# Kernel tuning notes

Hardware: AMD Instinct MI355X
Metric: run time of the kernel (lower is better)

## Reference

```python
import jax, jax.numpy as jnp
import numpy as np


def _gather_neighbours(h, idx):
    # h: (B, N, H); idx: (B, N, K) int -> (B, N, K, H)
    B, N, H = h.shape
    K = idx.shape[-1]
    flat = idx.reshape(B, N * K)  # (B, N*K)
    rep = jnp.take_along_axis(h, flat[..., None], axis=1)  # (B, N*K, H)
    return rep.reshape(B, N, K, H)


def _masked_agg(h, idx, mask):
    # gather neighbor hidden states then masked sum over neighbors -> (B, N, H)
    rep = _gather_neighbours(h, idx)
    return jnp.einsum('bnkh,bnk->bnh', rep, mask)


def setup_inputs() -> dict:
    key = jax.random.key(0)
    ks = jax.random.split(key, 12)
    B, N, H, K = 8, 2000, 128, 32
    s = 1.0 / np.sqrt(H)
    return {
        'node_hidden': jax.random.normal(ks[0], (B, N, H), jnp.float32),
        'cell': jax.random.normal(ks[1], (B, N, H), jnp.float32),
        'w_in': jax.random.normal(ks[2], (4, H, H), jnp.float32) * s,
        'w_out': jax.random.normal(ks[3], (4, H, H), jnp.float32) * s,
        'u_in': jax.random.normal(ks[4], (4, H, H), jnp.float32) * s,
        'u_out': jax.random.normal(ks[5], (4, H, H), jnp.float32) * s,
        'b': jax.random.normal(ks[6], (4, H), jnp.float32) * 0.1,
        'in_node_mask': jax.random.uniform(ks[7], (B, N, K), jnp.float32),
        'out_node_mask': jax.random.uniform(ks[8], (B, N, K), jnp.float32),
        'in_node_index': jax.random.randint(ks[9], (B, N, K), 0, N, jnp.int32),
        'out_node_index': jax.random.randint(ks[10], (B, N, K), 0, N, jnp.int32),
        'layer_num': 2,
    }


def reference(node_hidden, cell, w_in, w_out, u_in, u_out, b,
              in_node_mask, out_node_mask, in_node_index, out_node_index,
              layer_num):
    h, c = node_hidden, cell
    for _ in range(layer_num):
        in_agg = _masked_agg(h, in_node_index, in_node_mask)    # (B,N,H)
        out_agg = _masked_agg(h, out_node_index, out_node_mask)  # (B,N,H)
        # gate pre-activations, gate order: i, o, f, cell
        pre = (jnp.einsum('bnh,ghd->gbnd', in_agg, w_in)
               + jnp.einsum('bnh,ghd->gbnd', out_agg, w_out)
               + jnp.einsum('bnh,ghd->gbnd', h, u_in)
               + jnp.einsum('bnh,ghd->gbnd', h, u_out)
               + b[:, None, None, :])
        i_g = jax.nn.sigmoid(pre[0])
        o_g = jax.nn.sigmoid(pre[1])
        f_g = jax.nn.sigmoid(pre[2])
        g = jnp.tanh(pre[3])
        c = f_g * c + i_g * g
        h = o_g * jnp.tanh(c)
    return h
```

## Files before the change

kernel.cpp:

```cpp
#include <hip/hip_runtime.h>
#include <math.h>

#define B_ 8
#define N_ 2000
#define H_ 128
#define K_ 32
#define M_ (B_*N_)
#define KTOT 384
#define NC 512
#define NTILES 32
#define NCHUNK 12
#define ACHUNK 8

typedef __attribute__((ext_vector_type(8))) short s8_t;
typedef __attribute__((ext_vector_type(4))) float f4_t;

__device__ __forceinline__ unsigned short f2bf(float x) {
    union { float f; unsigned u; } v; v.f = x;
    unsigned r = v.u + 0x7fff + ((v.u >> 16) & 1);
    return (unsigned short)(r >> 16);
}
__device__ __forceinline__ float bf2f(unsigned short b) {
    union { unsigned u; float f; } v; v.u = (unsigned)b << 16; return v.f;
}
__device__ __forceinline__ float sigm_(float x) { return 1.f / (1.f + __expf(-x)); }
__device__ __forceinline__ float tanh_(float x) { return 2.f / (1.f + __expf(-2.f * x)) - 1.f; }

__device__ __forceinline__ float pickv(f4_t A, int m) {
    float ab = (m & 1) ? A.y : A.x;
    float cd = (m & 1) ? A.w : A.z;
    return (m & 2) ? cd : ab;
}
__device__ __forceinline__ float pick4(float u0, float u1, float u2, float u3, int m) {
    float ab = (m & 1) ? u1 : u0;
    float cd = (m & 1) ? u3 : u2;
    return (m & 2) ? cd : ab;
}

__global__ __launch_bounds__(512)
void prep_kernel(const float* __restrict__ w_in,
                 const float* __restrict__ w_out,
                 const float* __restrict__ u_in,
                 const float* __restrict__ u_out,
                 unsigned short* __restrict__ wp_hi,
                 unsigned short* __restrict__ wp_lo) {
    int blk = blockIdx.x;
    int ntile = blk / NCHUNK, chunk = blk % NCHUNK;
    int t = threadIdx.x;
    int lane = t >> 3, e = t & 7;
    int col = ntile * 16 + (lane & 15);
    int k = chunk * 32 + (lane >> 4) * 8 + e;
    int d = col >> 2, g = col & 3;
    float v;
    if (k < 128) {
        v = w_in[(g * 128 + k) * 128 + d];
    } else if (k < 256) {
        v = w_out[(g * 128 + (k - 128)) * 128 + d];
    } else {
        int kk = k - 256;
        v = u_in[(g * 128 + kk) * 128 + d] + u_out[(g * 128 + kk) * 128 + d];
    }
    unsigned short hs = f2bf(v);
    wp_hi[(size_t)blk * 512 + t] = hs;
    wp_lo[(size_t)blk * 512 + t] = f2bf(v - bf2f(hs));
}

__global__ __launch_bounds__(256)
void agg_kernel(const float* __restrict__ h,
                const int* __restrict__ in_idx,
                const float* __restrict__ in_mask,
                const int* __restrict__ out_idx,
                const float* __restrict__ out_mask,
                unsigned short* __restrict__ A_hi,
                unsigned short* __restrict__ A_lo) {
    int tid = threadIdx.x;
    int r = tid >> 5;
    int p = tid & 31;
    int row = blockIdx.x * 8 + r;
    int b = row / N_;
    const float* hb = h + (size_t)b * N_ * H_;

    __shared__ int   s_idx[8][64];
    __shared__ float s_msk[8][64];
    for (int e = tid; e < 512; e += 256) {
        int r2 = e >> 6, q = e & 63;
        int ridx = blockIdx.x * 8 + r2;
        if (q < 32) {
            s_idx[r2][q] = in_idx[ridx * K_ + q];
            s_msk[r2][q] = in_mask[ridx * K_ + q];
        } else {
            s_idx[r2][q] = out_idx[ridx * K_ + (q - 32)];
            s_msk[r2][q] = out_mask[ridx * K_ + (q - 32)];
        }
    }
    __syncthreads();

    int d0 = p * 4;
    float ai[4] = {0.f, 0.f, 0.f, 0.f};
    float ao[4] = {0.f, 0.f, 0.f, 0.f};
    #pragma unroll 4
    for (int k = 0; k < K_; ++k) {
        int   i1 = s_idx[r][k];
        float m1 = s_msk[r][k];
        int   i2 = s_idx[r][32 + k];
        float m2 = s_msk[r][32 + k];
        float4 v1 = *(const float4*)(hb + (size_t)i1 * H_ + d0);
        float4 v2 = *(const float4*)(hb + (size_t)i2 * H_ + d0);
        ai[0] += m1 * v1.x; ai[1] += m1 * v1.y; ai[2] += m1 * v1.z; ai[3] += m1 * v1.w;
        ao[0] += m2 * v2.x; ao[1] += m2 * v2.y; ao[2] += m2 * v2.z; ao[3] += m2 * v2.w;
    }

    int mtile = row >> 4;
    int kg = (p >> 1) & 3;
    int e0 = (p & 1) * 4;
    int lane = (row & 15) + 16 * kg;
    size_t bi = ((size_t)(mtile * ACHUNK + (p >> 3)) * 64 + lane) * 8 + e0;
    size_t bo = ((size_t)(mtile * ACHUNK + 4 + (p >> 3)) * 64 + lane) * 8 + e0;

    ushort4 hi_i, lo_i, hi_o, lo_o;
    {
        unsigned short h0 = f2bf(ai[0]), h1 = f2bf(ai[1]), h2 = f2bf(ai[2]), h3 = f2bf(ai[3]);
        hi_i = make_ushort4(h0, h1, h2, h3);
        lo_i = make_ushort4(f2bf(ai[0] - bf2f(h0)), f2bf(ai[1] - bf2f(h1)),
                            f2bf(ai[2] - bf2f(h2)), f2bf(ai[3] - bf2f(h3)));
        unsigned short g0 = f2bf(ao[0]), g1 = f2bf(ao[1]), g2 = f2bf(ao[2]), g3 = f2bf(ao[3]);
        hi_o = make_ushort4(g0, g1, g2, g3);
        lo_o = make_ushort4(f2bf(ao[0] - bf2f(g0)), f2bf(ao[1] - bf2f(g1)),
                            f2bf(ao[2] - bf2f(g2)), f2bf(ao[3] - bf2f(g3)));
    }
    *(ushort4*)(A_hi + bi) = hi_i;
    *(ushort4*)(A_lo + bi) = lo_i;
    *(ushort4*)(A_hi + bo) = hi_o;
    *(ushort4*)(A_lo + bo) = lo_o;
}

__global__ __launch_bounds__(256, 4)
void gemm_gates(const unsigned short* __restrict__ A_hi,
                const unsigned short* __restrict__ A_lo,
                const float* __restrict__ h_src,
                const unsigned short* __restrict__ wp_hi,
                const unsigned short* __restrict__ wp_lo,
                const float* __restrict__ bias,
                const float* __restrict__ c_src,
                float* __restrict__ c_dst,
                float* __restrict__ h_dst,
                int write_c) {
    int tid  = threadIdx.x;
    int mt   = blockIdx.x;
    int jt   = blockIdx.y;
    int lane = tid & 63;
    int w    = tid >> 6;
    int row0 = mt * 64;
    int m_off = (w & 1) * 32;
    int n_off = (w >> 1) * 64;
    int ml = lane & 15;
    int kg = lane >> 4;

    int mtile0 = mt * 4 + (w & 1) * 2;
    int ntile0 = jt * 8 + (w >> 1) * 4;

    f4_t zero = {0.f, 0.f, 0.f, 0.f};
    f4_t acc[2][4];
    #pragma unroll
    for (int i = 0; i < 2; ++i)
        #pragma unroll
        for (int j = 0; j < 4; ++j) acc[i][j] = zero;

    #pragma unroll 1
    for (int c = 0; c < ACHUNK; ++c) {
        s8_t a_hi[2], a_lo[2], b_hi[4], b_lo[4];
        #pragma unroll
        for (int i = 0; i < 2; ++i) {
            size_t off = ((size_t)((mtile0 + i) * ACHUNK + c) * 64 + lane) * 8;
            a_hi[i] = *(const s8_t*)(A_hi + off);
            a_lo[i] = *(const s8_t*)(A_lo + off);
        }
        #pragma unroll
        for (int j = 0; j < 4; ++j) {
            size_t boff = ((size_t)((ntile0 + j) * NCHUNK + c) * 64 + lane) * 8;
            b_hi[j] = *(const s8_t*)(wp_hi + boff);
            b_lo[j] = *(const s8_t*)(wp_lo + boff);
        }
        #pragma unroll
        for (int i = 0; i < 2; ++i)
            #pragma unroll
            for (int j = 0; j < 4; ++j) {
                acc[i][j] = __builtin_amdgcn_mfma_f32_16x16x32_bf16(a_hi[i], b_hi[j], acc[i][j], 0, 0, 0);
                acc[i][j] = __builtin_amdgcn_mfma_f32_16x16x32_bf16(a_hi[i], b_lo[j], acc[i][j], 0, 0, 0);
                acc[i][j] = __builtin_amdgcn_mfma_f32_16x16x32_bf16(a_lo[i], b_hi[j], acc[i][j], 0, 0, 0);
            }
    }

    #pragma unroll 1
    for (int c = ACHUNK; c < NCHUNK; ++c) {
        s8_t a_hi[2], a_lo[2], b_hi[4], b_lo[4];
        #pragma unroll
        for (int i = 0; i < 2; ++i) {
            const float* ph = h_src + (size_t)(row0 + m_off + i * 16 + ml) * H_
                              + (c - ACHUNK) * 32 + kg * 8;
            float4 f0 = *(const float4*)ph;
            float4 f1 = *(const float4*)(ph + 4);
            float fv[8] = {f0.x, f0.y, f0.z, f0.w, f1.x, f1.y, f1.z, f1.w};
            s8_t hv, lv;
            #pragma unroll
            for (int e = 0; e < 8; ++e) {
                unsigned short hs = f2bf(fv[e]);
                hv[e] = (short)hs;
                lv[e] = (short)f2bf(fv[e] - bf2f(hs));
            }
            a_hi[i] = hv;
            a_lo[i] = lv;
        }
        #pragma unroll
        for (int j = 0; j < 4; ++j) {
            size_t boff = ((size_t)((ntile0 + j) * NCHUNK + c) * 64 + lane) * 8;
            b_hi[j] = *(const s8_t*)(wp_hi + boff);
            b_lo[j] = *(const s8_t*)(wp_lo + boff);
        }
        #pragma unroll
        for (int i = 0; i < 2; ++i)
            #pragma unroll
            for (int j = 0; j < 4; ++j) {
                acc[i][j] = __builtin_amdgcn_mfma_f32_16x16x32_bf16(a_hi[i], b_hi[j], acc[i][j], 0, 0, 0);
                acc[i][j] = __builtin_amdgcn_mfma_f32_16x16x32_bf16(a_hi[i], b_lo[j], acc[i][j], 0, 0, 0);
                acc[i][j] = __builtin_amdgcn_mfma_f32_16x16x32_bf16(a_lo[i], b_hi[j], acc[i][j], 0, 0, 0);
            }
    }

    int g    = lane & 3;
    int qrow = lane >> 4;
    int dl   = (lane >> 2) & 3;
    #pragma unroll
    for (int j = 0; j < 4; ++j) {
        int ncol_base = jt * 128 + n_off + j * 16;
        int d = (ncol_base >> 2) + dl;
        float b0 = bias[0 * 128 + d];
        float b1 = bias[1 * 128 + d];
        float b2 = bias[2 * 128 + d];
        float b3 = bias[3 * 128 + d];
        #pragma unroll
        for (int i = 0; i < 2; ++i) {
            f4_t A = acc[i][j];
            float s0 = pickv(A, g);
            float s1 = pickv(A, g ^ 1);
            float s2 = pickv(A, g ^ 2);
            float s3 = pickv(A, g ^ 3);
            float u0 = s0;
            float u1 = __shfl_xor(s1, 1);
            float u2 = __shfl_xor(s2, 2);
            float u3 = __shfl_xor(s3, 3);
            float p0 = pick4(u0, u1, u2, u3, g) + b0;
            float p1 = pick4(u0, u1, u2, u3, g ^ 1) + b1;
            float p2 = pick4(u0, u1, u2, u3, g ^ 2) + b2;
            float p3 = pick4(u0, u1, u2, u3, g ^ 3) + b3;
            float ig = sigm_(p0);
            float og = sigm_(p1);
            float fg = sigm_(p2);
            float cg = tanh_(p3);
            int row = row0 + m_off + i * 16 + qrow * 4 + g;
            size_t off = (size_t)row * H_ + d;
            float c_old = c_src[off];
            float c_new = fg * c_old + ig * cg;
            if (write_c) c_dst[off] = c_new;
            h_dst[off] = og * tanh_(c_new);
        }
    }
}

extern "C" void kernel_launch(void* const* d_in, const int* in_sizes, int n_in,
                              void* d_out, int out_size, void* d_ws, size_t ws_size,
                              hipStream_t stream) {
    const float* node_hidden = (const float*)d_in[0];
    const float* cell        = (const float*)d_in[1];
    const float* w_in        = (const float*)d_in[2];
    const float* w_out       = (const float*)d_in[3];
    const float* u_in        = (const float*)d_in[4];
    const float* u_out       = (const float*)d_in[5];
    const float* bias        = (const float*)d_in[6];
    const float* in_mask     = (const float*)d_in[7];
    const float* out_mask    = (const float*)d_in[8];
    const int*   in_idx      = (const int*)d_in[9];
    const int*   out_idx     = (const int*)d_in[10];
    float* out = (float*)d_out;

    char* p = (char*)d_ws;
    unsigned short* wp_hi = (unsigned short*)p; p += (size_t)NTILES * NCHUNK * 512 * 2;
    unsigned short* wp_lo = (unsigned short*)p; p += (size_t)NTILES * NCHUNK * 512 * 2;
    unsigned short* A_hi  = (unsigned short*)p; p += (size_t)(M_/16) * ACHUNK * 512 * 2;
    unsigned short* A_lo  = (unsigned short*)p; p += (size_t)(M_/16) * ACHUNK * 512 * 2;
    float* h_buf = (float*)p;                   p += (size_t)M_ * H_ * 4;

    prep_kernel<<<NTILES * NCHUNK, 512, 0, stream>>>(w_in, w_out, u_in, u_out, wp_hi, wp_lo);

    agg_kernel<<<M_ / 8, 256, 0, stream>>>(node_hidden, in_idx, in_mask,
                                           out_idx, out_mask, A_hi, A_lo);
    gemm_gates<<<dim3(M_ / 64, 4), 256, 0, stream>>>(
        A_hi, A_lo, node_hidden, wp_hi, wp_lo, bias, cell, out, h_buf, 1);

    agg_kernel<<<M_ / 8, 256, 0, stream>>>(h_buf, in_idx, in_mask,
                                           out_idx, out_mask, A_hi, A_lo);
    gemm_gates<<<dim3(M_ / 64, 4), 256, 0, stream>>>(
        A_hi, A_lo, h_buf, wp_hi, wp_lo, bias, out, out, out, 0);
}
```

Measured before the change: 210.0 us.

## Pre-split h into packed A operand and double-buffer GEMM loads

The aggregation kernel now also converts each node's own hidden state into the packed bf16 hi/lo A layout, so the GEMM reads all 12 K-chunks from one packed buffer instead of converting fp32 h inline. The GEMM loop is fully unrolled with two register buffers so the next chunk's loads are issued before the current chunk's MFMAs, and the occupancy hint in launch_bounds is dropped. The aggregation block index is also remapped (blockIdx & 7) * 250 + (blockIdx >> 3), which spreads consecutive blocks across batches, presumably to balance gather traffic across XCD caches. The cost is a larger packed A buffer written and read through memory, and more registers per GEMM thread.

New measurement: 207.2 us. Within noise of the previous version (-1.4%).

```diff
diff --git a/kernel.cpp b/kernel.cpp
--- a/kernel.cpp
+++ b/kernel.cpp
@@ -10,7 +10,6 @@
 #define NC 512
 #define NTILES 32
 #define NCHUNK 12
-#define ACHUNK 8
 
 typedef __attribute__((ext_vector_type(8))) short s8_t;
 typedef __attribute__((ext_vector_type(4))) float f4_t;
@@ -35,6 +34,13 @@
     float ab = (m & 1) ? u1 : u0;
     float cd = (m & 1) ? u3 : u2;
     return (m & 2) ? cd : ab;
+}
+
+__device__ __forceinline__ void split4(const float* f, ushort4& hi, ushort4& lo) {
+    unsigned short h0 = f2bf(f[0]), h1 = f2bf(f[1]), h2 = f2bf(f[2]), h3 = f2bf(f[3]);
+    hi = make_ushort4(h0, h1, h2, h3);
+    lo = make_ushort4(f2bf(f[0] - bf2f(h0)), f2bf(f[1] - bf2f(h1)),
+                      f2bf(f[2] - bf2f(h2)), f2bf(f[3] - bf2f(h3)));
 }
 
 __global__ __launch_bounds__(512)
@@ -73,10 +79,11 @@
                 const float* __restrict__ out_mask,
                 unsigned short* __restrict__ A_hi,
                 unsigned short* __restrict__ A_lo) {
+    int bid = (blockIdx.x & 7) * 250 + (blockIdx.x >> 3);
     int tid = threadIdx.x;
     int r = tid >> 5;
     int p = tid & 31;
-    int row = blockIdx.x * 8 + r;
+    int row = bid * 8 + r;
     int b = row / N_;
     const float* hb = h + (size_t)b * N_ * H_;
 
@@ -84,7 +91,7 @@
     __shared__ float s_msk[8][64];
     for (int e = tid; e < 512; e += 256) {
         int r2 = e >> 6, q = e & 63;
-        int ridx = blockIdx.x * 8 + r2;
+        int ridx = bid * 8 + r2;
         if (q < 32) {
             s_idx[r2][q] = in_idx[ridx * K_ + q];
             s_msk[r2][q] = in_mask[ridx * K_ + q];
@@ -109,35 +116,26 @@
         ai[0] += m1 * v1.x; ai[1] += m1 * v1.y; ai[2] += m1 * v1.z; ai[3] += m1 * v1.w;
         ao[0] += m2 * v2.x; ao[1] += m2 * v2.y; ao[2] += m2 * v2.z; ao[3] += m2 * v2.w;
     }
+    float4 hv4 = *(const float4*)(h + (size_t)row * H_ + d0);
+    float hh[4] = {hv4.x, hv4.y, hv4.z, hv4.w};
 
     int mtile = row >> 4;
     int kg = (p >> 1) & 3;
     int e0 = (p & 1) * 4;
     int lane = (row & 15) + 16 * kg;
-    size_t bi = ((size_t)(mtile * ACHUNK + (p >> 3)) * 64 + lane) * 8 + e0;
-    size_t bo = ((size_t)(mtile * ACHUNK + 4 + (p >> 3)) * 64 + lane) * 8 + e0;
-
-    ushort4 hi_i, lo_i, hi_o, lo_o;
-    {
-        unsigned short h0 = f2bf(ai[0]), h1 = f2bf(ai[1]), h2 = f2bf(ai[2]), h3 = f2bf(ai[3]);
-        hi_i = make_ushort4(h0, h1, h2, h3);
-        lo_i = make_ushort4(f2bf(ai[0] - bf2f(h0)), f2bf(ai[1] - bf2f(h1)),
-                            f2bf(ai[2] - bf2f(h2)), f2bf(ai[3] - bf2f(h3)));
-        unsigned short g0 = f2bf(ao[0]), g1 = f2bf(ao[1]), g2 = f2bf(ao[2]), g3 = f2bf(ao[3]);
-        hi_o = make_ushort4(g0, g1, g2, g3);
-        lo_o = make_ushort4(f2bf(ao[0] - bf2f(g0)), f2bf(ao[1] - bf2f(g1)),
-                            f2bf(ao[2] - bf2f(g2)), f2bf(ao[3] - bf2f(g3)));
-    }
-    *(ushort4*)(A_hi + bi) = hi_i;
-    *(ushort4*)(A_lo + bi) = lo_i;
-    *(ushort4*)(A_hi + bo) = hi_o;
-    *(ushort4*)(A_lo + bo) = lo_o;
-}
-
-__global__ __launch_bounds__(256, 4)
+    size_t bi = ((size_t)(mtile * NCHUNK +     (p >> 3)) * 64 + lane) * 8 + e0;
+    size_t bo = ((size_t)(mtile * NCHUNK + 4 + (p >> 3)) * 64 + lane) * 8 + e0;
+    size_t bh = ((size_t)(mtile * NCHUNK + 8 + (p >> 3)) * 64 + lane) * 8 + e0;
+
+    ushort4 hi, lo;
+    split4(ai, hi, lo); *(ushort4*)(A_hi + bi) = hi; *(ushort4*)(A_lo + bi) = lo;
+    split4(ao, hi, lo); *(ushort4*)(A_hi + bo) = hi; *(ushort4*)(A_lo + bo) = lo;
+    split4(hh, hi, lo); *(ushort4*)(A_hi + bh) = hi; *(ushort4*)(A_lo + bh) = lo;
+}
+
+__global__ __launch_bounds__(256)
 void gemm_gates(const unsigned short* __restrict__ A_hi,
                 const unsigned short* __restrict__ A_lo,
-                const float* __restrict__ h_src,
                 const unsigned short* __restrict__ wp_hi,
                 const unsigned short* __restrict__ wp_lo,
                 const float* __restrict__ bias,
@@ -153,11 +151,16 @@
     int row0 = mt * 64;
     int m_off = (w & 1) * 32;
     int n_off = (w >> 1) * 64;
-    int ml = lane & 15;
-    int kg = lane >> 4;
 
     int mtile0 = mt * 4 + (w & 1) * 2;
     int ntile0 = jt * 8 + (w >> 1) * 4;
+
+    const unsigned short* pa0 = A_hi + ((size_t)mtile0 * NCHUNK * 64 + lane) * 8;
+    const unsigned short* pa1 = A_lo + ((size_t)mtile0 * NCHUNK * 64 + lane) * 8;
+    const unsigned short* pb0 = wp_hi + ((size_t)ntile0 * NCHUNK * 64 + lane) * 8;
+    const unsigned short* pb1 = wp_lo + ((size_t)ntile0 * NCHUNK * 64 + lane) * 8;
+    const size_t mstride = (size_t)NCHUNK * 512;
+    const size_t cstride = 512;
 
     f4_t zero = {0.f, 0.f, 0.f, 0.f};
     f4_t acc[2][4];
@@ -166,66 +169,45 @@
         #pragma unroll
         for (int j = 0; j < 4; ++j) acc[i][j] = zero;
 
-    #pragma unroll 1
-    for (int c = 0; c < ACHUNK; ++c) {
-        s8_t a_hi[2], a_lo[2], b_hi[4], b_lo[4];
-        #pragma unroll
-        for (int i = 0; i < 2; ++i) {
-            size_t off = ((size_t)((mtile0 + i) * ACHUNK + c) * 64 + lane) * 8;
-            a_hi[i] = *(const s8_t*)(A_hi + off);
-            a_lo[i] = *(const s8_t*)(A_lo + off);
-        }
-        #pragma unroll
-        for (int j = 0; j < 4; ++j) {
-            size_t boff = ((size_t)((ntile0 + j) * NCHUNK + c) * 64 + lane) * 8;
-            b_hi[j] = *(const s8_t*)(wp_hi + boff);
-            b_lo[j] = *(const s8_t*)(wp_lo + boff);
-        }
-        #pragma unroll
-        for (int i = 0; i < 2; ++i)
-            #pragma unroll
-            for (int j = 0; j < 4; ++j) {
-                acc[i][j] = __builtin_amdgcn_mfma_f32_16x16x32_bf16(a_hi[i], b_hi[j], acc[i][j], 0, 0, 0);
-                acc[i][j] = __builtin_amdgcn_mfma_f32_16x16x32_bf16(a_hi[i], b_lo[j], acc[i][j], 0, 0, 0);
-                acc[i][j] = __builtin_amdgcn_mfma_f32_16x16x32_bf16(a_lo[i], b_hi[j], acc[i][j], 0, 0, 0);
-            }
-    }
-
-    #pragma unroll 1
-    for (int c = ACHUNK; c < NCHUNK; ++c) {
-        s8_t a_hi[2], a_lo[2], b_hi[4], b_lo[4];
-        #pragma unroll
-        for (int i = 0; i < 2; ++i) {
-            const float* ph = h_src + (size_t)(row0 + m_off + i * 16 + ml) * H_
-                              + (c - ACHUNK) * 32 + kg * 8;
-            float4 f0 = *(const float4*)ph;
-            float4 f1 = *(const float4*)(ph + 4);
-            float fv[8] = {f0.x, f0.y, f0.z, f0.w, f1.x, f1.y, f1.z, f1.w};
-            s8_t hv, lv;
-            #pragma unroll
-            for (int e = 0; e < 8; ++e) {
-                unsigned short hs = f2bf(fv[e]);
-                hv[e] = (short)hs;
-                lv[e] = (short)f2bf(fv[e] - bf2f(hs));
-            }
-            a_hi[i] = hv;
-            a_lo[i] = lv;
-        }
-        #pragma unroll
-        for (int j = 0; j < 4; ++j) {
-            size_t boff = ((size_t)((ntile0 + j) * NCHUNK + c) * 64 + lane) * 8;
-            b_hi[j] = *(const s8_t*)(wp_hi + boff);
-            b_lo[j] = *(const s8_t*)(wp_lo + boff);
-        }
-        #pragma unroll
-        for (int i = 0; i < 2; ++i)
-            #pragma unroll
-            for (int j = 0; j < 4; ++j) {
-                acc[i][j] = __builtin_amdgcn_mfma_f32_16x16x32_bf16(a_hi[i], b_hi[j], acc[i][j], 0, 0, 0);
-                acc[i][j] = __builtin_amdgcn_mfma_f32_16x16x32_bf16(a_hi[i], b_lo[j], acc[i][j], 0, 0, 0);
-                acc[i][j] = __builtin_amdgcn_mfma_f32_16x16x32_bf16(a_lo[i], b_hi[j], acc[i][j], 0, 0, 0);
-            }
-    }
+    s8_t ahA[2], alA[2], bhA[4], blA[4];
+    s8_t ahB[2], alB[2], bhB[4], blB[4];
+
+#define LOADF(ah, al, bh, bl, c)                                              \
+    {                                                                         \
+        _Pragma("unroll")                                                     \
+        for (int i = 0; i < 2; ++i) {                                         \
+            ah[i] = *(const s8_t*)(pa0 + i * mstride + (c) * cstride);        \
+            al[i] = *(const s8_t*)(pa1 + i * mstride + (c) * cstride);        \
+        }                                                                     \
+        _Pragma("unroll")                                                     \
+        for (int j = 0; j < 4; ++j) {                                         \
+            bh[j] = *(const s8_t*)(pb0 + j * mstride + (c) * cstride);        \
+            bl[j] = *(const s8_t*)(pb1 + j * mstride + (c) * cstride);        \
+        }                                                                     \
+    }
+
+#define MFMAF(ah, al, bh, bl)                                                 \
+    {                                                                         \
+        _Pragma("unroll")                                                     \
+        for (int i = 0; i < 2; ++i)                                           \
+            _Pragma("unroll")                                                 \
+            for (int j = 0; j < 4; ++j) {                                     \
+                acc[i][j] = __builtin_amdgcn_mfma_f32_16x16x32_bf16(ah[i], bh[j], acc[i][j], 0, 0, 0); \
+                acc[i][j] = __builtin_amdgcn_mfma_f32_16x16x32_bf16(ah[i], bl[j], acc[i][j], 0, 0, 0); \
+                acc[i][j] = __builtin_amdgcn_mfma_f32_16x16x32_bf16(al[i], bh[j], acc[i][j], 0, 0, 0); \
+            }                                                                 \
+    }
+
+    LOADF(ahA, alA, bhA, blA, 0)
+    #pragma unroll
+    for (int c = 0; c < NCHUNK; c += 2) {
+        LOADF(ahB, alB, bhB, blB, c + 1)
+        MFMAF(ahA, alA, bhA, blA)
+        if (c + 2 < NCHUNK) LOADF(ahA, alA, bhA, blA, c + 2)
+        MFMAF(ahB, alB, bhB, blB)
+    }
+#undef LOADF
+#undef MFMAF
 
     int g    = lane & 3;
     int qrow = lane >> 4;
@@ -286,8 +268,8 @@
     char* p = (char*)d_ws;
     unsigned short* wp_hi = (unsigned short*)p; p += (size_t)NTILES * NCHUNK * 512 * 2;
     unsigned short* wp_lo = (unsigned short*)p; p += (size_t)NTILES * NCHUNK * 512 * 2;
-    unsigned short* A_hi  = (unsigned short*)p; p += (size_t)(M_/16) * ACHUNK * 512 * 2;
-    unsigned short* A_lo  = (unsigned short*)p; p += (size_t)(M_/16) * ACHUNK * 512 * 2;
+    unsigned short* A_hi  = (unsigned short*)p; p += (size_t)(M_/16) * NCHUNK * 512 * 2;
+    unsigned short* A_lo  = (unsigned short*)p; p += (size_t)(M_/16) * NCHUNK * 512 * 2;
     float* h_buf = (float*)p;                   p += (size_t)M_ * H_ * 4;
 
     prep_kernel<<<NTILES * NCHUNK, 512, 0, stream>>>(w_in, w_out, u_in, u_out, wp_hi, wp_lo);
@@ -295,10 +277,10 @@
     agg_kernel<<<M_ / 8, 256, 0, stream>>>(node_hidden, in_idx, in_mask,
                                            out_idx, out_mask, A_hi, A_lo);
     gemm_gates<<<dim3(M_ / 64, 4), 256, 0, stream>>>(
-        A_hi, A_lo, node_hidden, wp_hi, wp_lo, bias, cell, out, h_buf, 1);
+        A_hi, A_lo, wp_hi, wp_lo, bias, cell, out, h_buf, 1);
 
     agg_kernel<<<M_ / 8, 256, 0, stream>>>(h_buf, in_idx, in_mask,
                                            out_idx, out_mask, A_hi, A_lo);
     gemm_gates<<<dim3(M_ / 64, 4), 256, 0, stream>>>(
-        A_hi, A_lo, h_buf, wp_hi, wp_lo, bias, out, out, out, 0);
-}
+        A_hi, A_lo, wp_hi, wp_lo, bias, out, out, out, 0);
+}
```
